# Kernel optimization log

Hardware: AMD Instinct MI355X
Metric: run time of the kernel (lower is better)

## Reference

```python
import jax, jax.numpy as jnp
import numpy as np

EPS = 0.1
B, D, H = 1048576, 2, 64


def _lagrangian(xs, W0, b0, W1, b1, W2, b2, W3, b3):
    # xs: [2] single sample -> scalar Lagrangian L(q, v)
    h = jnp.tanh(xs @ W0 + b0)
    h = jnp.tanh(h @ W1 + b1)
    h = jnp.tanh(h @ W2 + b2)
    return (h @ W3 + b3)[0]


def setup_inputs() -> dict:
    key = jax.random.key(0)
    ks = jax.random.split(key, 9)
    def lin(k, fan_in, fan_out):
        # mimic nn.Linear default init U(-1/sqrt(fan_in), 1/sqrt(fan_in))
        bound = 1.0 / np.sqrt(fan_in)
        kw, kb = jax.random.split(k)
        W = jax.random.uniform(kw, (fan_in, fan_out), jnp.float32, -bound, bound)
        b = jax.random.uniform(kb, (fan_out,), jnp.float32, -bound, bound)
        return W, b
    W0, b0 = lin(ks[1], D, H)
    W1, b1 = lin(ks[2], H, H)
    W2, b2 = lin(ks[3], H, H)
    W3, b3 = lin(ks[4], H, 1)
    x = jax.random.normal(ks[0], (B, D), jnp.float32)
    return {"t": 0, "x": x, "W0": W0, "b0": b0, "W1": W1, "b1": b1,
            "W2": W2, "b2": b2, "W3": W3, "b3": b3}


def reference(t, x, W0, b0, W1, b1, W2, b2, W3, b3):
    lag = lambda xs: _lagrangian(xs, W0, b0, W1, b1, W2, b2, W3, b3)
    grad_all = jax.vmap(jax.grad(lag))(x)          # [B, 2]
    H_full = jax.vmap(jax.hessian(lag))(x)          # [B, 2, 2]
    dL_dq = grad_all[:, 0:1]                        # [B, 1]
    d2L_dqv = H_full[:, 1, 0:1]                     # d2L/(dv dq)
    d2L_dv2 = H_full[:, 1, 1:2]                     # d2L/dv2
    v = x[:, 1:2]
    a = (dL_dq - d2L_dqv * v) / (d2L_dv2 + EPS)
    return jnp.concatenate([v, a], axis=1)          # [B, 2]
```

## Files before the change

kernel.cpp:

```cpp
#include <hip/hip_runtime.h>
#include <hip/hip_fp16.h>

typedef _Float16 half8 __attribute__((ext_vector_type(8)));
typedef float    f32x4 __attribute__((ext_vector_type(4)));
typedef float    f32x2 __attribute__((ext_vector_type(2)));

#define EPSL 0.1f
#define TWO_LOG2E 2.8853900817779268f

#if __has_builtin(__builtin_amdgcn_exp2f)
#define EXP2(x) __builtin_amdgcn_exp2f(x)
#else
#define EXP2(x) __expf((x) * 0.6931471805599453f)
#endif

__device__ __forceinline__ f32x2 tanh2s(f32x2 y) {
    f32x2 e;
    e.x = EXP2(y.x);
    e.y = EXP2(y.y);
    const f32x2 ep = e + 1.0f;
    f32x2 r;
    r.x = __builtin_amdgcn_rcpf(ep.x);
    r.y = __builtin_amdgcn_rcpf(ep.y);
    return 1.0f - 2.0f * r;
}

__device__ __forceinline__ unsigned int pk2(float a, float b) {
    union { __fp16 __attribute__((ext_vector_type(2))) h; unsigned int u; } v;
    v.h = __builtin_amdgcn_cvt_pkrtz(a, b);
    return v.u;
}
__device__ __forceinline__ f32x2 unpk2v(unsigned int u) {
    union { unsigned int u; __half2 h; } v; v.u = u;
    const float2 f = __half22float2(v.h);
    return (f32x2){f.x, f.y};
}
__device__ __forceinline__ f32x2 lo2(f32x4 v) { return __builtin_shufflevector(v, v, 0, 1); }
__device__ __forceinline__ f32x2 hi2(f32x4 v) { return __builtin_shufflevector(v, v, 2, 3); }

union frag_u { unsigned int u[4]; half8 h; };

__global__ void pack_weights(const float* __restrict__ W1,
                             const float* __restrict__ W2,
                             _Float16* __restrict__ pk) {
    const int t = threadIdx.x;
    const int combo = blockIdx.x;
    const int mt  = combo & 3;
    const int kt  = (combo >> 2) & 1;
    const int mat = combo >> 3;
    const int q = t >> 4, r = t & 15;
    _Float16 v[8];
    #pragma unroll
    for (int j = 0; j < 8; ++j) {
        const int fk = (2 * kt + (j >> 2)) * 16 + 4 * q + (j & 3);
        float x;
        if (mat == 0)      x = W1[(kt * 32 + 8 * q + j) * 64 + mt * 16 + r];
        else if (mat == 1) x = W2[fk * 64 + mt * 16 + r];
        else if (mat == 2) x = W2[(mt * 16 + r) * 64 + fk];
        else {
            const int f0 = (mt & 1) * 32 + 8 * (r >> 2) + ((mt >> 1) & 1) * 4 + (r & 3);
            x = W1[f0 * 64 + fk];
        }
        v[j] = (_Float16)x;
    }
    *(half8*)(pk + combo * 512 + t * 8) = *(const half8*)v;
}

extern "C" __global__ void __launch_bounds__(256)
lnn_mfma(const float* __restrict__ x,
         const float* __restrict__ W0, const float* __restrict__ b0,
         const float* __restrict__ b1, const float* __restrict__ b2,
         const float* __restrict__ W3,
         const _Float16* __restrict__ pk,
         float* __restrict__ out)
{
    const int t = threadIdx.x & 63;
    const int q = t >> 4;
    const int r = t & 15;
    const long sbase = (long)blockIdx.x * 64 + (threadIdx.x >> 6) * 16;

    const float2 xv = *(const float2*)(x + 2 * (sbase + r));
    const float x0 = xv.x, x1 = xv.y;

    auto ldpk = [&](int mat, int kt, int mt) -> half8 {
        return *(const half8*)(pk + ((mat * 2 + kt) * 4 + mt) * 512 + t * 8);
    };

    half8 ah0[2], at0[2];
    #pragma unroll
    for (int kt = 0; kt < 2; ++kt) {
        const int f = kt * 32 + q * 8;
        const float4 waA = *(const float4*)(W0 + f);
        const float4 waB = *(const float4*)(W0 + f + 4);
        const float4 wbA = *(const float4*)(W0 + 64 + f);
        const float4 wbB = *(const float4*)(W0 + 64 + f + 4);
        const float4 bbA = *(const float4*)(b0 + f);
        const float4 bbB = *(const float4*)(b0 + f + 4);
        const f32x2 wa2[4] = {{waA.x,waA.y},{waA.z,waA.w},{waB.x,waB.y},{waB.z,waB.w}};
        const f32x2 wb2[4] = {{wbA.x,wbA.y},{wbA.z,wbA.w},{wbB.x,wbB.y},{wbB.z,wbB.w}};
        const f32x2 bb2[4] = {{bbA.x,bbA.y},{bbA.z,bbA.w},{bbB.x,bbB.y},{bbB.z,bbB.w}};
        union { unsigned int u[4]; half8 h; } ph, pt;
        #pragma unroll
        for (int p = 0; p < 4; ++p) {
            const f32x2 z = x0 * wa2[p] + x1 * wb2[p] + bb2[p];
            const f32x2 h = tanh2s(z * TWO_LOG2E);
            const f32x2 A = 1.0f - h * h;
            const f32x2 tt = A * wb2[p];
            ph.u[p] = pk2(h.x, h.y);
            pt.u[p] = pk2(tt.x, tt.y);
        }
        ah0[kt] = ph.h; at0[kt] = pt.h;
    }

    f32x4 acc[4], tacc[4];
    #pragma unroll
    for (int mt = 0; mt < 4; ++mt) {
        acc[mt]  = *(const f32x4*)(b1 + mt * 16 + 4 * q);
        tacc[mt] = (f32x4){0, 0, 0, 0};
    }
    #pragma unroll
    for (int kt = 0; kt < 2; ++kt)
        #pragma unroll
        for (int mt = 0; mt < 4; ++mt) {
            const half8 aw = ldpk(0, kt, mt);
            acc[mt]  = __builtin_amdgcn_mfma_f32_16x16x32_f16(aw, ah0[kt], acc[mt], 0, 0, 0);
            tacc[mt] = __builtin_amdgcn_mfma_f32_16x16x32_f16(aw, at0[kt], tacc[mt], 0, 0, 0);
        }

    frag_u bh1[2], bt1[2];
    #pragma unroll
    for (int mt = 0; mt < 4; ++mt) {
        const f32x2 zp[2] = {lo2(acc[mt]),  hi2(acc[mt])};
        const f32x2 tp[2] = {lo2(tacc[mt]), hi2(tacc[mt])};
        #pragma unroll
        for (int p = 0; p < 2; ++p) {
            const f32x2 h  = tanh2s(zp[p] * TWO_LOG2E);
            const f32x2 A  = 1.0f - h * h;
            const f32x2 th = A * tp[p];
            bh1[mt >> 1].u[2 * (mt & 1) + p] = pk2(h.x, h.y);
            bt1[mt >> 1].u[2 * (mt & 1) + p] = pk2(th.x, th.y);
        }
    }

    #pragma unroll
    for (int mt = 0; mt < 4; ++mt) {
        acc[mt]  = *(const f32x4*)(b2 + mt * 16 + 4 * q);
        tacc[mt] = (f32x4){0, 0, 0, 0};
    }
    #pragma unroll
    for (int kt = 0; kt < 2; ++kt)
        #pragma unroll
        for (int mt = 0; mt < 4; ++mt) {
            const half8 aw = ldpk(1, kt, mt);
            acc[mt]  = __builtin_amdgcn_mfma_f32_16x16x32_f16(aw, bh1[kt].h, acc[mt], 0, 0, 0);
            tacc[mt] = __builtin_amdgcn_mfma_f32_16x16x32_f16(aw, bt1[kt].h, tacc[mt], 0, 0, 0);
        }

    frag_u bh2[2], bt2[2];
    #pragma unroll
    for (int mt = 0; mt < 4; ++mt) {
        const float4 w3v = *(const float4*)(W3 + mt * 16 + 4 * q);
        const f32x2 w3p[2] = {{w3v.x, w3v.y}, {w3v.z, w3v.w}};
        const f32x2 zp[2] = {lo2(acc[mt]),  hi2(acc[mt])};
        const f32x2 tp[2] = {lo2(tacc[mt]), hi2(tacc[mt])};
        #pragma unroll
        for (int p = 0; p < 2; ++p) {
            const f32x2 h  = tanh2s(zp[p] * TWO_LOG2E);
            const f32x2 A  = 1.0f - h * h;
            const f32x2 dz = A * w3p[p];
            const f32x2 t1 = h * tp[p];
            const f32x2 td = -2.0f * (dz * t1);
            bh2[mt >> 1].u[2 * (mt & 1) + p] = pk2(dz.x, dz.y);
            bt2[mt >> 1].u[2 * (mt & 1) + p] = pk2(td.x, td.y);
        }
    }

    #pragma unroll
    for (int mt = 0; mt < 4; ++mt) { acc[mt] = (f32x4){0,0,0,0}; tacc[mt] = (f32x4){0,0,0,0}; }
    #pragma unroll
    for (int kt = 0; kt < 2; ++kt)
        #pragma unroll
        for (int mt = 0; mt < 4; ++mt) {
            const half8 aw = ldpk(2, kt, mt);
            acc[mt]  = __builtin_amdgcn_mfma_f32_16x16x32_f16(aw, bh2[kt].h, acc[mt], 0, 0, 0);
            tacc[mt] = __builtin_amdgcn_mfma_f32_16x16x32_f16(aw, bt2[kt].h, tacc[mt], 0, 0, 0);
        }

    frag_u bd[2], btd[2];
    #pragma unroll
    for (int mt = 0; mt < 4; ++mt) {
        const f32x2 gp[2] = {lo2(acc[mt]),  hi2(acc[mt])};
        const f32x2 tp[2] = {lo2(tacc[mt]), hi2(tacc[mt])};
        #pragma unroll
        for (int p = 0; p < 2; ++p) {
            const f32x2 h  = unpk2v(bh1[mt >> 1].u[2 * (mt & 1) + p]);
            const f32x2 th = unpk2v(bt1[mt >> 1].u[2 * (mt & 1) + p]);
            const f32x2 A  = 1.0f - h * h;
            const f32x2 d1 = gp[p] * A;
            const f32x2 u2 = (gp[p] * h) * th;
            const f32x2 td = tp[p] * A + (-2.0f) * u2;
            bd[mt >> 1].u[2 * (mt & 1) + p]  = pk2(d1.x, d1.y);
            btd[mt >> 1].u[2 * (mt & 1) + p] = pk2(td.x, td.y);
        }
    }

    #pragma unroll
    for (int mt = 0; mt < 4; ++mt) { acc[mt] = (f32x4){0,0,0,0}; tacc[mt] = (f32x4){0,0,0,0}; }
    #pragma unroll
    for (int kt = 0; kt < 2; ++kt)
        #pragma unroll
        for (int mt = 0; mt < 4; ++mt) {
            const half8 aw = ldpk(3, kt, mt);
            acc[mt]  = __builtin_amdgcn_mfma_f32_16x16x32_f16(aw, bd[kt].h,  acc[mt], 0, 0, 0);
            tacc[mt] = __builtin_amdgcn_mfma_f32_16x16x32_f16(aw, btd[kt].h, tacc[mt], 0, 0, 0);
        }

    f32x2 pg2 = {0, 0}, ph02 = {0, 0}, ph12 = {0, 0};
    #pragma unroll
    for (int mt = 0; mt < 4; ++mt) {
        const int kt = mt & 1;
        const int jb = ((mt >> 1) & 1) * 4;
        const int f  = kt * 32 + q * 8 + jb;
        const float4 waF = *(const float4*)(W0 + f);
        const float4 wbF = *(const float4*)(W0 + 64 + f);
        const f32x2 wa2[2] = {{waF.x, waF.y}, {waF.z, waF.w}};
        const f32x2 wb2[2] = {{wbF.x, wbF.y}, {wbF.z, wbF.w}};
        union { half8 h; unsigned int u[4]; } av; av.h = ah0[kt];
        const unsigned int hu[2] = {av.u[jb >> 1], av.u[(jb >> 1) + 1]};
        const f32x2 gp[2] = {lo2(acc[mt]),  hi2(acc[mt])};
        const f32x2 tp[2] = {lo2(tacc[mt]), hi2(tacc[mt])};
        #pragma unroll
        for (int p = 0; p < 2; ++p) {
            const f32x2 h   = unpk2v(hu[p]);
            const f32x2 A   = 1.0f - h * h;
            const f32x2 th0 = A * wb2[p];
            const f32x2 d0  = gp[p] * A;
            const f32x2 u2  = (gp[p] * h) * th0;
            const f32x2 td0 = tp[p] * A + (-2.0f) * u2;
            pg2  += wa2[p] * d0;
            ph02 += wa2[p] * td0;
            ph12 += wb2[p] * td0;
        }
    }
    float pg  = pg2.x  + pg2.y;
    float ph0 = ph02.x + ph02.y;
    float ph1 = ph12.x + ph12.y;
    pg  += __shfl_xor(pg, 16);  pg  += __shfl_xor(pg, 32);
    ph0 += __shfl_xor(ph0, 16); ph0 += __shfl_xor(ph0, 32);
    ph1 += __shfl_xor(ph1, 16); ph1 += __shfl_xor(ph1, 32);
    if (q == 0) {
        const float num = fmaf(-ph0, x1, pg);
        const float den = ph1 + EPSL;
        const float a = num * __builtin_amdgcn_rcpf(den);
        float2 o;
        o.x = x1;
        o.y = a;
        *(float2*)(out + 2 * (sbase + r)) = o;
    }
}

extern "C" void kernel_launch(void* const* d_in, const int* in_sizes, int n_in,
                              void* d_out, int out_size, void* d_ws, size_t ws_size,
                              hipStream_t stream) {
    const float* x  = (const float*)d_in[1];
    const float* W0 = (const float*)d_in[2];
    const float* b0 = (const float*)d_in[3];
    const float* W1 = (const float*)d_in[4];
    const float* b1 = (const float*)d_in[5];
    const float* W2 = (const float*)d_in[6];
    const float* b2 = (const float*)d_in[7];
    const float* W3 = (const float*)d_in[8];

    _Float16* pk = (_Float16*)d_ws;
    const int B = in_sizes[1] / 2;

    pack_weights<<<32, 64, 0, stream>>>(W1, W2, pk);
    lnn_mfma<<<B / 64, 256, 0, stream>>>(x, W0, b0, b1, b2, W3, pk, (float*)d_out);
}
```

Before: 228.0 us.

## Process two 16-sample tiles per wave and cap occupancy with LDS padding

Each wave now handles 32 samples as two independent 16-sample tiles. The packed weight fragments loaded for each MFMA are reused across both tiles, and the two independent MFMA chains give more instruction-level parallelism. A dummy 36 KB shared array, touched only on an impossible branch, limits how many blocks fit per CU to offset the higher register use. The grid is halved to match. The cost is roughly double the accumulator and fragment registers per thread, which could cause spills or lower occupancy.

```diff
diff --git a/kernel.cpp b/kernel.cpp
--- a/kernel.cpp
+++ b/kernel.cpp
@@ -74,19 +74,24 @@
          const _Float16* __restrict__ pk,
          float* __restrict__ out)
 {
+    __shared__ float occ_pad[9216];
+    if (blockIdx.x == 0xFFFFFFFFu) ((volatile float*)occ_pad)[threadIdx.x] = 1.0f;
+
     const int t = threadIdx.x & 63;
     const int q = t >> 4;
     const int r = t & 15;
-    const long sbase = (long)blockIdx.x * 64 + (threadIdx.x >> 6) * 16;
-
-    const float2 xv = *(const float2*)(x + 2 * (sbase + r));
-    const float x0 = xv.x, x1 = xv.y;
+    const long sbase = (long)blockIdx.x * 128 + (threadIdx.x >> 6) * 32;
+
+    const float2 xvA = *(const float2*)(x + 2 * (sbase + r));
+    const float2 xvB = *(const float2*)(x + 2 * (sbase + 16 + r));
+    const float x0v[2] = {xvA.x, xvB.x};
+    const float x1v[2] = {xvA.y, xvB.y};
 
     auto ldpk = [&](int mat, int kt, int mt) -> half8 {
         return *(const half8*)(pk + ((mat * 2 + kt) * 4 + mt) * 512 + t * 8);
     };
 
-    half8 ah0[2], at0[2];
+    half8 ah0[2][2], at0[2][2];
     #pragma unroll
     for (int kt = 0; kt < 2; ++kt) {
         const int f = kt * 32 + q * 8;
@@ -99,123 +104,153 @@
         const f32x2 wa2[4] = {{waA.x,waA.y},{waA.z,waA.w},{waB.x,waB.y},{waB.z,waB.w}};
         const f32x2 wb2[4] = {{wbA.x,wbA.y},{wbA.z,wbA.w},{wbB.x,wbB.y},{wbB.z,wbB.w}};
         const f32x2 bb2[4] = {{bbA.x,bbA.y},{bbA.z,bbA.w},{bbB.x,bbB.y},{bbB.z,bbB.w}};
-        union { unsigned int u[4]; half8 h; } ph, pt;
-        #pragma unroll
-        for (int p = 0; p < 4; ++p) {
-            const f32x2 z = x0 * wa2[p] + x1 * wb2[p] + bb2[p];
-            const f32x2 h = tanh2s(z * TWO_LOG2E);
-            const f32x2 A = 1.0f - h * h;
-            const f32x2 tt = A * wb2[p];
-            ph.u[p] = pk2(h.x, h.y);
-            pt.u[p] = pk2(tt.x, tt.y);
-        }
-        ah0[kt] = ph.h; at0[kt] = pt.h;
-    }
-
-    f32x4 acc[4], tacc[4];
+        #pragma unroll
+        for (int u = 0; u < 2; ++u) {
+            union { unsigned int uu[4]; half8 h; } ph, pt;
+            #pragma unroll
+            for (int p = 0; p < 4; ++p) {
+                const f32x2 z = x0v[u] * wa2[p] + x1v[u] * wb2[p] + bb2[p];
+                const f32x2 h = tanh2s(z * TWO_LOG2E);
+                const f32x2 A = 1.0f - h * h;
+                const f32x2 tt = A * wb2[p];
+                ph.uu[p] = pk2(h.x, h.y);
+                pt.uu[p] = pk2(tt.x, tt.y);
+            }
+            ah0[u][kt] = ph.h; at0[u][kt] = pt.h;
+        }
+    }
+
+    f32x4 acc[2][4], tacc[2][4];
     #pragma unroll
     for (int mt = 0; mt < 4; ++mt) {
-        acc[mt]  = *(const f32x4*)(b1 + mt * 16 + 4 * q);
-        tacc[mt] = (f32x4){0, 0, 0, 0};
+        const f32x4 bv = *(const f32x4*)(b1 + mt * 16 + 4 * q);
+        acc[0][mt] = bv;  acc[1][mt] = bv;
+        tacc[0][mt] = (f32x4){0,0,0,0};  tacc[1][mt] = (f32x4){0,0,0,0};
     }
     #pragma unroll
     for (int kt = 0; kt < 2; ++kt)
         #pragma unroll
         for (int mt = 0; mt < 4; ++mt) {
             const half8 aw = ldpk(0, kt, mt);
-            acc[mt]  = __builtin_amdgcn_mfma_f32_16x16x32_f16(aw, ah0[kt], acc[mt], 0, 0, 0);
-            tacc[mt] = __builtin_amdgcn_mfma_f32_16x16x32_f16(aw, at0[kt], tacc[mt], 0, 0, 0);
-        }
-
-    frag_u bh1[2], bt1[2];
+            #pragma unroll
+            for (int u = 0; u < 2; ++u) {
+                acc[u][mt]  = __builtin_amdgcn_mfma_f32_16x16x32_f16(aw, ah0[u][kt], acc[u][mt], 0, 0, 0);
+                tacc[u][mt] = __builtin_amdgcn_mfma_f32_16x16x32_f16(aw, at0[u][kt], tacc[u][mt], 0, 0, 0);
+            }
+        }
+
+    frag_u bh1[2][2], bt1[2][2];
+    #pragma unroll
+    for (int u = 0; u < 2; ++u)
+        #pragma unroll
+        for (int mt = 0; mt < 4; ++mt) {
+            const f32x2 zp[2] = {lo2(acc[u][mt]),  hi2(acc[u][mt])};
+            const f32x2 tp[2] = {lo2(tacc[u][mt]), hi2(tacc[u][mt])};
+            #pragma unroll
+            for (int p = 0; p < 2; ++p) {
+                const f32x2 h  = tanh2s(zp[p] * TWO_LOG2E);
+                const f32x2 A  = 1.0f - h * h;
+                const f32x2 th = A * tp[p];
+                bh1[u][mt >> 1].u[2 * (mt & 1) + p] = pk2(h.x, h.y);
+                bt1[u][mt >> 1].u[2 * (mt & 1) + p] = pk2(th.x, th.y);
+            }
+        }
+
     #pragma unroll
     for (int mt = 0; mt < 4; ++mt) {
-        const f32x2 zp[2] = {lo2(acc[mt]),  hi2(acc[mt])};
-        const f32x2 tp[2] = {lo2(tacc[mt]), hi2(tacc[mt])};
-        #pragma unroll
-        for (int p = 0; p < 2; ++p) {
-            const f32x2 h  = tanh2s(zp[p] * TWO_LOG2E);
-            const f32x2 A  = 1.0f - h * h;
-            const f32x2 th = A * tp[p];
-            bh1[mt >> 1].u[2 * (mt & 1) + p] = pk2(h.x, h.y);
-            bt1[mt >> 1].u[2 * (mt & 1) + p] = pk2(th.x, th.y);
-        }
-    }
-
-    #pragma unroll
-    for (int mt = 0; mt < 4; ++mt) {
-        acc[mt]  = *(const f32x4*)(b2 + mt * 16 + 4 * q);
-        tacc[mt] = (f32x4){0, 0, 0, 0};
+        const f32x4 bv = *(const f32x4*)(b2 + mt * 16 + 4 * q);
+        acc[0][mt] = bv;  acc[1][mt] = bv;
+        tacc[0][mt] = (f32x4){0,0,0,0};  tacc[1][mt] = (f32x4){0,0,0,0};
     }
     #pragma unroll
     for (int kt = 0; kt < 2; ++kt)
         #pragma unroll
         for (int mt = 0; mt < 4; ++mt) {
             const half8 aw = ldpk(1, kt, mt);
-            acc[mt]  = __builtin_amdgcn_mfma_f32_16x16x32_f16(aw, bh1[kt].h, acc[mt], 0, 0, 0);
-            tacc[mt] = __builtin_amdgcn_mfma_f32_16x16x32_f16(aw, bt1[kt].h, tacc[mt], 0, 0, 0);
-        }
-
-    frag_u bh2[2], bt2[2];
+            #pragma unroll
+            for (int u = 0; u < 2; ++u) {
+                acc[u][mt]  = __builtin_amdgcn_mfma_f32_16x16x32_f16(aw, bh1[u][kt].h, acc[u][mt], 0, 0, 0);
+                tacc[u][mt] = __builtin_amdgcn_mfma_f32_16x16x32_f16(aw, bt1[u][kt].h, tacc[u][mt], 0, 0, 0);
+            }
+        }
+
+    frag_u bh2[2][2], bt2[2][2];
     #pragma unroll
     for (int mt = 0; mt < 4; ++mt) {
         const float4 w3v = *(const float4*)(W3 + mt * 16 + 4 * q);
         const f32x2 w3p[2] = {{w3v.x, w3v.y}, {w3v.z, w3v.w}};
-        const f32x2 zp[2] = {lo2(acc[mt]),  hi2(acc[mt])};
-        const f32x2 tp[2] = {lo2(tacc[mt]), hi2(tacc[mt])};
-        #pragma unroll
-        for (int p = 0; p < 2; ++p) {
-            const f32x2 h  = tanh2s(zp[p] * TWO_LOG2E);
-            const f32x2 A  = 1.0f - h * h;
-            const f32x2 dz = A * w3p[p];
-            const f32x2 t1 = h * tp[p];
-            const f32x2 td = -2.0f * (dz * t1);
-            bh2[mt >> 1].u[2 * (mt & 1) + p] = pk2(dz.x, dz.y);
-            bt2[mt >> 1].u[2 * (mt & 1) + p] = pk2(td.x, td.y);
-        }
-    }
-
-    #pragma unroll
-    for (int mt = 0; mt < 4; ++mt) { acc[mt] = (f32x4){0,0,0,0}; tacc[mt] = (f32x4){0,0,0,0}; }
+        #pragma unroll
+        for (int u = 0; u < 2; ++u) {
+            const f32x2 zp[2] = {lo2(acc[u][mt]),  hi2(acc[u][mt])};
+            const f32x2 tp[2] = {lo2(tacc[u][mt]), hi2(tacc[u][mt])};
+            #pragma unroll
+            for (int p = 0; p < 2; ++p) {
+                const f32x2 h  = tanh2s(zp[p] * TWO_LOG2E);
+                const f32x2 A  = 1.0f - h * h;
+                const f32x2 dz = A * w3p[p];
+                const f32x2 t1 = h * tp[p];
+                const f32x2 td = -2.0f * (dz * t1);
+                bh2[u][mt >> 1].u[2 * (mt & 1) + p] = pk2(dz.x, dz.y);
+                bt2[u][mt >> 1].u[2 * (mt & 1) + p] = pk2(td.x, td.y);
+            }
+        }
+    }
+
+    #pragma unroll
+    for (int u = 0; u < 2; ++u)
+        #pragma unroll
+        for (int mt = 0; mt < 4; ++mt) { acc[u][mt] = (f32x4){0,0,0,0}; tacc[u][mt] = (f32x4){0,0,0,0}; }
     #pragma unroll
     for (int kt = 0; kt < 2; ++kt)
         #pragma unroll
         for (int mt = 0; mt < 4; ++mt) {
             const half8 aw = ldpk(2, kt, mt);
-            acc[mt]  = __builtin_amdgcn_mfma_f32_16x16x32_f16(aw, bh2[kt].h, acc[mt], 0, 0, 0);
-            tacc[mt] = __builtin_amdgcn_mfma_f32_16x16x32_f16(aw, bt2[kt].h, tacc[mt], 0, 0, 0);
-        }
-
-    frag_u bd[2], btd[2];
-    #pragma unroll
-    for (int mt = 0; mt < 4; ++mt) {
-        const f32x2 gp[2] = {lo2(acc[mt]),  hi2(acc[mt])};
-        const f32x2 tp[2] = {lo2(tacc[mt]), hi2(tacc[mt])};
-        #pragma unroll
-        for (int p = 0; p < 2; ++p) {
-            const f32x2 h  = unpk2v(bh1[mt >> 1].u[2 * (mt & 1) + p]);
-            const f32x2 th = unpk2v(bt1[mt >> 1].u[2 * (mt & 1) + p]);
-            const f32x2 A  = 1.0f - h * h;
-            const f32x2 d1 = gp[p] * A;
-            const f32x2 u2 = (gp[p] * h) * th;
-            const f32x2 td = tp[p] * A + (-2.0f) * u2;
-            bd[mt >> 1].u[2 * (mt & 1) + p]  = pk2(d1.x, d1.y);
-            btd[mt >> 1].u[2 * (mt & 1) + p] = pk2(td.x, td.y);
-        }
-    }
-
-    #pragma unroll
-    for (int mt = 0; mt < 4; ++mt) { acc[mt] = (f32x4){0,0,0,0}; tacc[mt] = (f32x4){0,0,0,0}; }
+            #pragma unroll
+            for (int u = 0; u < 2; ++u) {
+                acc[u][mt]  = __builtin_amdgcn_mfma_f32_16x16x32_f16(aw, bh2[u][kt].h, acc[u][mt], 0, 0, 0);
+                tacc[u][mt] = __builtin_amdgcn_mfma_f32_16x16x32_f16(aw, bt2[u][kt].h, tacc[u][mt], 0, 0, 0);
+            }
+        }
+
+    frag_u bd[2][2], btd[2][2];
+    #pragma unroll
+    for (int u = 0; u < 2; ++u)
+        #pragma unroll
+        for (int mt = 0; mt < 4; ++mt) {
+            const f32x2 gp[2] = {lo2(acc[u][mt]),  hi2(acc[u][mt])};
+            const f32x2 tp[2] = {lo2(tacc[u][mt]), hi2(tacc[u][mt])};
+            #pragma unroll
+            for (int p = 0; p < 2; ++p) {
+                const f32x2 h  = unpk2v(bh1[u][mt >> 1].u[2 * (mt & 1) + p]);
+                const f32x2 th = unpk2v(bt1[u][mt >> 1].u[2 * (mt & 1) + p]);
+                const f32x2 A  = 1.0f - h * h;
+                const f32x2 d1 = gp[p] * A;
+                const f32x2 u2 = (gp[p] * h) * th;
+                const f32x2 td = tp[p] * A + (-2.0f) * u2;
+                bd[u][mt >> 1].u[2 * (mt & 1) + p]  = pk2(d1.x, d1.y);
+                btd[u][mt >> 1].u[2 * (mt & 1) + p] = pk2(td.x, td.y);
+            }
+        }
+
+    #pragma unroll
+    for (int u = 0; u < 2; ++u)
+        #pragma unroll
+        for (int mt = 0; mt < 4; ++mt) { acc[u][mt] = (f32x4){0,0,0,0}; tacc[u][mt] = (f32x4){0,0,0,0}; }
     #pragma unroll
     for (int kt = 0; kt < 2; ++kt)
         #pragma unroll
         for (int mt = 0; mt < 4; ++mt) {
             const half8 aw = ldpk(3, kt, mt);
-            acc[mt]  = __builtin_amdgcn_mfma_f32_16x16x32_f16(aw, bd[kt].h,  acc[mt], 0, 0, 0);
-            tacc[mt] = __builtin_amdgcn_mfma_f32_16x16x32_f16(aw, btd[kt].h, tacc[mt], 0, 0, 0);
-        }
-
-    f32x2 pg2 = {0, 0}, ph02 = {0, 0}, ph12 = {0, 0};
+            #pragma unroll
+            for (int u = 0; u < 2; ++u) {
+                acc[u][mt]  = __builtin_amdgcn_mfma_f32_16x16x32_f16(aw, bd[u][kt].h,  acc[u][mt], 0, 0, 0);
+                tacc[u][mt] = __builtin_amdgcn_mfma_f32_16x16x32_f16(aw, btd[u][kt].h, tacc[u][mt], 0, 0, 0);
+            }
+        }
+
+    f32x2 pg2[2]  = {{0,0},{0,0}};
+    f32x2 ph02[2] = {{0,0},{0,0}};
+    f32x2 ph12[2] = {{0,0},{0,0}};
     #pragma unroll
     for (int mt = 0; mt < 4; ++mt) {
         const int kt = mt & 1;
@@ -225,37 +260,43 @@
         const float4 wbF = *(const float4*)(W0 + 64 + f);
         const f32x2 wa2[2] = {{waF.x, waF.y}, {waF.z, waF.w}};
         const f32x2 wb2[2] = {{wbF.x, wbF.y}, {wbF.z, wbF.w}};
-        union { half8 h; unsigned int u[4]; } av; av.h = ah0[kt];
-        const unsigned int hu[2] = {av.u[jb >> 1], av.u[(jb >> 1) + 1]};
-        const f32x2 gp[2] = {lo2(acc[mt]),  hi2(acc[mt])};
-        const f32x2 tp[2] = {lo2(tacc[mt]), hi2(tacc[mt])};
-        #pragma unroll
-        for (int p = 0; p < 2; ++p) {
-            const f32x2 h   = unpk2v(hu[p]);
-            const f32x2 A   = 1.0f - h * h;
-            const f32x2 th0 = A * wb2[p];
-            const f32x2 d0  = gp[p] * A;
-            const f32x2 u2  = (gp[p] * h) * th0;
-            const f32x2 td0 = tp[p] * A + (-2.0f) * u2;
-            pg2  += wa2[p] * d0;
-            ph02 += wa2[p] * td0;
-            ph12 += wb2[p] * td0;
-        }
-    }
-    float pg  = pg2.x  + pg2.y;
-    float ph0 = ph02.x + ph02.y;
-    float ph1 = ph12.x + ph12.y;
-    pg  += __shfl_xor(pg, 16);  pg  += __shfl_xor(pg, 32);
-    ph0 += __shfl_xor(ph0, 16); ph0 += __shfl_xor(ph0, 32);
-    ph1 += __shfl_xor(ph1, 16); ph1 += __shfl_xor(ph1, 32);
-    if (q == 0) {
-        const float num = fmaf(-ph0, x1, pg);
-        const float den = ph1 + EPSL;
-        const float a = num * __builtin_amdgcn_rcpf(den);
-        float2 o;
-        o.x = x1;
-        o.y = a;
-        *(float2*)(out + 2 * (sbase + r)) = o;
+        #pragma unroll
+        for (int u = 0; u < 2; ++u) {
+            union { half8 h; unsigned int uu[4]; } av; av.h = ah0[u][kt];
+            const unsigned int hu[2] = {av.uu[jb >> 1], av.uu[(jb >> 1) + 1]};
+            const f32x2 gp[2] = {lo2(acc[u][mt]),  hi2(acc[u][mt])};
+            const f32x2 tp[2] = {lo2(tacc[u][mt]), hi2(tacc[u][mt])};
+            #pragma unroll
+            for (int p = 0; p < 2; ++p) {
+                const f32x2 h   = unpk2v(hu[p]);
+                const f32x2 A   = 1.0f - h * h;
+                const f32x2 th0 = A * wb2[p];
+                const f32x2 d0  = gp[p] * A;
+                const f32x2 u2  = (gp[p] * h) * th0;
+                const f32x2 td0 = tp[p] * A + (-2.0f) * u2;
+                pg2[u]  += wa2[p] * d0;
+                ph02[u] += wa2[p] * td0;
+                ph12[u] += wb2[p] * td0;
+            }
+        }
+    }
+    #pragma unroll
+    for (int u = 0; u < 2; ++u) {
+        float pg  = pg2[u].x  + pg2[u].y;
+        float ph0 = ph02[u].x + ph02[u].y;
+        float ph1 = ph12[u].x + ph12[u].y;
+        pg  += __shfl_xor(pg, 16);  pg  += __shfl_xor(pg, 32);
+        ph0 += __shfl_xor(ph0, 16); ph0 += __shfl_xor(ph0, 32);
+        ph1 += __shfl_xor(ph1, 16); ph1 += __shfl_xor(ph1, 32);
+        if (q == 0) {
+            const float num = fmaf(-ph0, x1v[u], pg);
+            const float den = ph1 + EPSL;
+            const float a = num * __builtin_amdgcn_rcpf(den);
+            float2 o;
+            o.x = x1v[u];
+            o.y = a;
+            *(float2*)(out + 2 * (sbase + u * 16 + r)) = o;
+        }
     }
 }
 
@@ -275,5 +316,5 @@
     const int B = in_sizes[1] / 2;
 
     pack_weights<<<32, 64, 0, stream>>>(W1, W2, pk);
-    lnn_mfma<<<B / 64, 256, 0, stream>>>(x, W0, b0, b1, b2, W3, pk, (float*)d_out);
-}
+    lnn_mfma<<<B / 128, 256, 0, stream>>>(x, W0, b0, b1, b2, W3, pk, (float*)d_out);
+}
```

After: 202.4 us. 1.13x faster.
